# Performance work log

Hardware: AMD Instinct MI355X
Metric: run time of the kernel (lower is better)

Reference implementation:

```python
import jax, jax.numpy as jnp
import numpy as np

B, S, D, H = 8, 1024, 256, 8
DH = D // H
NEG = -1e32


def setup_inputs() -> dict:
    key = jax.random.key(0)
    ks = jax.random.split(key, 8)
    scale = 1.0 / np.sqrt(D)
    return {
        "q": jax.random.normal(ks[0], (B, S, D), jnp.float32),
        "k": jax.random.normal(ks[1], (B, S, D), jnp.float32),
        "v": jax.random.normal(ks[2], (B, S, D), jnp.float32),
        "mask": jnp.tril(jnp.ones((1, 1, S, S), dtype=bool)),
        "Wq": jax.random.normal(ks[3], (D, D), jnp.float32) * scale,
        "bq": jnp.zeros((D,), jnp.float32),
        "Wv": jax.random.normal(ks[4], (D, D), jnp.float32) * scale,
        "bv": jnp.zeros((D,), jnp.float32),
        "Wo": jax.random.normal(ks[5], (D, D), jnp.float32) * scale,
        "bo": jnp.zeros((D,), jnp.float32),
        "gammas": jax.random.normal(ks[6], (H, 1, 1), jnp.float32) * 0.1,
    }


def reference(q, k, v, mask, Wq, bq, Wv, bv, Wo, bo, gammas):
    def split_heads(x):  # [B,S,D] -> [B,H,S,DH]
        return x.reshape(B, S, H, DH).transpose(0, 2, 1, 3)

    # key_query_same=True: key projection shares query weights
    qh = split_heads(q @ Wq.T + bq)
    kh = split_heads(k @ Wq.T + bq)
    vh = split_heads(v @ Wv.T + bv)

    scores = jnp.einsum('bhqd,bhkd->bhqk', qh, kh) / jnp.sqrt(jnp.float32(DH))

    # distance-decay effect (computed on detached softmax of masked scores)
    sp = jax.nn.softmax(jnp.where(mask, scores, NEG), axis=-1)
    distcum = jnp.cumsum(sp, axis=-1)                      # [B,H,S,S]
    disttot = jnp.sum(sp, axis=-1, keepdims=True)          # [B,H,S,1]
    pos = jnp.abs(jnp.arange(S)[None, :] - jnp.arange(S)[:, None]).astype(jnp.float32)
    dist = jnp.sqrt(jnp.clip((disttot - distcum) * pos[None, None], 0.0, None))
    dist = jax.lax.stop_gradient(dist)

    g = -jnp.abs(gammas)[None]                             # [1,H,1,1]
    total_effect = jnp.clip(jnp.exp(g * dist), 1e-5, 1e5)

    scores = scores * total_effect
    scores = jax.nn.softmax(jnp.where(mask, scores, NEG), axis=-1)

    out = jnp.einsum('bhqk,bhkd->bhqd', scores, vh)
    concat = out.transpose(0, 2, 1, 3).reshape(B, S, D)
    output = concat @ Wo.T + bo
    return output, scores
```

## Files before the change

kernel.cpp:

```cpp
#include <hip/hip_runtime.h>
#include <hip/hip_fp16.h>
#include <math.h>

constexpr int Bsz = 8, Ssz = 1024, Dsz = 256, Hn = 8, DHn = 32;
constexpr int SST = 1160;

typedef __attribute__((ext_vector_type(8))) short short8;
typedef __attribute__((ext_vector_type(4))) float floatx4;

#define DEV static __device__ __forceinline__

DEV short f2bf(float f) {
  union { float f; unsigned u; } x; x.f = f;
  return (short)((x.u + 0x7fffu + ((x.u >> 16) & 1u)) >> 16);
}
DEV short f2h(float f) {
  __half h = __float2half(f);
  return *(short*)&h;
}
DEV float wmax(float v) {
#pragma unroll
  for (int off = 32; off > 0; off >>= 1) v = fmaxf(v, __shfl_xor(v, off, 64));
  return v;
}
DEV float wsum(float v) {
#pragma unroll
  for (int off = 32; off > 0; off >>= 1) v += __shfl_xor(v, off, 64);
  return v;
}
DEV float wscan_incl(float v) {
  float x = v;
  const int ln = threadIdx.x & 63;
#pragma unroll
  for (int off = 1; off < 64; off <<= 1) {
    float y = __shfl_up(x, off, 64);
    if (ln >= off) x += y;
  }
  return x;
}

DEV void stage_f32(const float* __restrict__ src, short* dst, int k0, int tid) {
  const int row = tid >> 2, cg = tid & 3;
#pragma unroll
  for (int i = 0; i < 4; ++i) {
    const float4 f = *(const float4*)(src + (size_t)row * 256 + k0 + cg * 16 + i * 4);
    const int g = cg * 2 + (i >> 1);
    const int pg = g ^ (row & 7);
    short4 s; s.x = f2bf(f.x); s.y = f2bf(f.y); s.z = f2bf(f.z); s.w = f2bf(f.w);
    *(short4*)(dst + row * 80 + pg * 8 + (i & 1) * 4) = s;
  }
}
DEV void stage_bf16(const short* __restrict__ src, short* dst, int k0, int tid) {
  const int row = tid >> 2, cg = tid & 3;
#pragma unroll
  for (int i = 0; i < 2; ++i) {
    const short8 s = *(const short8*)(src + (size_t)row * 256 + k0 + cg * 16 + i * 8);
    const int pg = (cg * 2 + i) ^ (row & 7);
    *(short8*)(dst + row * 80 + pg * 8) = s;
  }
}

__global__ __launch_bounds__(256, 4) void proj_qkv(
    const float* __restrict__ qi, const float* __restrict__ ki, const float* __restrict__ vi,
    const float* __restrict__ Wq, const float* __restrict__ bq,
    const float* __restrict__ Wv, const float* __restrict__ bv,
    short* __restrict__ qh, short* __restrict__ kh, short* __restrict__ vt) {
  __shared__ short As[64 * 80];
  __shared__ short Bs[64 * 80];
  const int which = blockIdx.y;
  const float* X = (which == 0) ? qi : (which == 1) ? ki : vi;
  const float* W = (which == 2) ? Wv : Wq;
  const float* bias = (which == 2) ? bv : bq;
  const int tid = threadIdx.x, ln = tid & 63, w = tid >> 6;
  const int lm = ln & 15, qq = ln >> 4;
  const int bm = blockIdx.x & 127, bn = blockIdx.x >> 7;
  const float* Xb = X + (size_t)bm * 64 * 256;
  const float* Wb = W + (size_t)bn * 64 * 256;
  const int moff = (w & 1) * 32, noff = (w >> 1) * 32;
  floatx4 acc[2][2] = {};

  for (int k0 = 0; k0 < 256; k0 += 64) {
    __syncthreads();
    stage_f32(Xb, As, k0, tid);
    stage_f32(Wb, Bs, k0, tid);
    __syncthreads();
#pragma unroll
    for (int ks = 0; ks < 2; ++ks) {
      short8 a[2], b[2];
#pragma unroll
      for (int mt = 0; mt < 2; ++mt) {
        const int row = moff + mt * 16 + lm;
        a[mt] = *(const short8*)(As + row * 80 + ((ks * 4 + qq) ^ (row & 7)) * 8);
      }
#pragma unroll
      for (int nt = 0; nt < 2; ++nt) {
        const int row = noff + nt * 16 + lm;
        b[nt] = *(const short8*)(Bs + row * 80 + ((ks * 4 + qq) ^ (row & 7)) * 8);
      }
#pragma unroll
      for (int mt = 0; mt < 2; ++mt)
#pragma unroll
        for (int nt = 0; nt < 2; ++nt)
          acc[mt][nt] = __builtin_amdgcn_mfma_f32_16x16x32_bf16(a[mt], b[nt], acc[mt][nt], 0, 0, 0);
    }
  }

  short* dst = (which == 0) ? qh : (which == 1) ? kh : vt;
#pragma unroll
  for (int mt = 0; mt < 2; ++mt) {
#pragma unroll
    for (int nt = 0; nt < 2; ++nt) {
      const int n = bn * 64 + noff + nt * 16 + lm;
      const float bval = bias[n];
      const int m0 = bm * 64 + moff + mt * 16 + qq * 4;
      const int h = n >> 5, dh = n & 31;
      if (which <= 1) {
#pragma unroll
        for (int r = 0; r < 4; ++r) {
          const int m = m0 + r, b_ = m >> 10, s = m & 1023;
          dst[(((size_t)(b_ * Hn + h) << 10) + s) * DHn + dh] = f2bf(acc[mt][nt][r] + bval);
        }
      } else {
        const int b_ = m0 >> 10, s0 = m0 & 1023;
        short4 pk;
        pk.x = f2bf(acc[mt][nt][0] + bval);
        pk.y = f2bf(acc[mt][nt][1] + bval);
        pk.z = f2bf(acc[mt][nt][2] + bval);
        pk.w = f2bf(acc[mt][nt][3] + bval);
        *(short4*)(dst + ((size_t)((b_ * Hn + h) * DHn + dh) << 10) + s0) = pk;
      }
    }
  }
}

__global__ __launch_bounds__(256, 4) void proj_out(
    const short* __restrict__ oc, const float* __restrict__ Wo,
    const float* __restrict__ bo, float* __restrict__ out) {
  __shared__ short As[64 * 80];
  __shared__ short Bs[64 * 80];
  const int tid = threadIdx.x, ln = tid & 63, w = tid >> 6;
  const int lm = ln & 15, qq = ln >> 4;
  const int bm = blockIdx.x & 127, bn = blockIdx.x >> 7;
  const short* Xb = oc + (size_t)bm * 64 * 256;
  const float* Wb = Wo + (size_t)bn * 64 * 256;
  const int moff = (w & 1) * 32, noff = (w >> 1) * 32;
  floatx4 acc[2][2] = {};

  for (int k0 = 0; k0 < 256; k0 += 64) {
    __syncthreads();
    stage_bf16(Xb, As, k0, tid);
    stage_f32(Wb, Bs, k0, tid);
    __syncthreads();
#pragma unroll
    for (int ks = 0; ks < 2; ++ks) {
      short8 a[2], b[2];
#pragma unroll
      for (int mt = 0; mt < 2; ++mt) {
        const int row = moff + mt * 16 + lm;
        a[mt] = *(const short8*)(As + row * 80 + ((ks * 4 + qq) ^ (row & 7)) * 8);
      }
#pragma unroll
      for (int nt = 0; nt < 2; ++nt) {
        const int row = noff + nt * 16 + lm;
        b[nt] = *(const short8*)(Bs + row * 80 + ((ks * 4 + qq) ^ (row & 7)) * 8);
      }
#pragma unroll
      for (int mt = 0; mt < 2; ++mt)
#pragma unroll
        for (int nt = 0; nt < 2; ++nt)
          acc[mt][nt] = __builtin_amdgcn_mfma_f32_16x16x32_bf16(a[mt], b[nt], acc[mt][nt], 0, 0, 0);
    }
  }
#pragma unroll
  for (int mt = 0; mt < 2; ++mt)
#pragma unroll
    for (int nt = 0; nt < 2; ++nt) {
      const int n = bn * 64 + noff + nt * 16 + lm;
      const float bval = bo[n];
      const int m0 = bm * 64 + moff + mt * 16 + qq * 4;
#pragma unroll
      for (int r = 0; r < 4; ++r)
        out[(size_t)(m0 + r) * 256 + n] = acc[mt][nt][r] + bval;
    }
}

template <int NP>
DEV void phase2(short* ss, float* shead, int row0, int w, int ln, float g) {
  const int c0 = ln * 4;
  for (int rr = 0; rr < 4; ++rr) {
    const int m = w * 4 + rr;
    const int irow = row0 + m;
    short* srow = ss + m * SST;

    float sv[NP * 4], e[NP * 4];
    float lm1 = -INFINITY;
#pragma unroll
    for (int p = 0; p < NP; ++p) {
      const uint2 u = *(const uint2*)(srow + p * 256 + c0);
      const float2 f0 = __half22float2(*(const __half2*)&u.x);
      const float2 f1 = __half22float2(*(const __half2*)&u.y);
      sv[p * 4 + 0] = f0.x; sv[p * 4 + 1] = f0.y;
      sv[p * 4 + 2] = f1.x; sv[p * 4 + 3] = f1.y;
#pragma unroll
      for (int j = 0; j < 4; ++j)
        if (p * 256 + c0 + j <= irow) lm1 = fmaxf(lm1, sv[p * 4 + j]);
    }
    const float m1 = wmax(lm1);

    float carry = 0.f, excl[NP];
#pragma unroll
    for (int p = 0; p < NP; ++p) {
      float ls = 0.f;
#pragma unroll
      for (int j = 0; j < 4; ++j) {
        const int c = p * 256 + c0 + j;
        e[p * 4 + j] = (c <= irow) ? __expf(sv[p * 4 + j] - m1) : 0.f;
        ls += e[p * 4 + j];
      }
      const float incl = wscan_incl(ls);
      excl[p] = carry + incl - ls;
      carry += __shfl(incl, 63, 64);
    }
    const float Z = carry, invZ = 1.f / Z;

    float lm2 = -INFINITY;
#pragma unroll
    for (int p = 0; p < NP; ++p) {
      float cum = excl[p];
#pragma unroll
      for (int j = 0; j < 4; ++j) {
        const int c = p * 256 + c0 + j;
        cum += e[p * 4 + j];
        const float tail = (Z - cum) * invZ;
        const float pos = (float)(irow - c);
        const float dist = sqrtf(fmaxf(tail * pos, 0.f));
        float eff = __expf(g * dist);
        eff = fminf(fmaxf(eff, 1e-5f), 1e5f);
        const float s2 = sv[p * 4 + j] * eff;
        sv[p * 4 + j] = s2;
        if (c <= irow) lm2 = fmaxf(lm2, s2);
      }
    }
    const float m2 = wmax(lm2);

    float ls2 = 0.f;
#pragma unroll
    for (int p = 0; p < NP; ++p)
#pragma unroll
      for (int j = 0; j < 4; ++j) {
        const int c = p * 256 + c0 + j;
        e[p * 4 + j] = (c <= irow) ? __expf(sv[p * 4 + j] - m2) : 0.f;
        ls2 += e[p * 4 + j];
      }
    const float i2 = 1.f / wsum(ls2);

    float* grow = shead + (size_t)irow * Ssz;
#pragma unroll
    for (int p = 0; p < NP; ++p) {
      float4 o;
      o.x = e[p * 4 + 0] * i2; o.y = e[p * 4 + 1] * i2;
      o.z = e[p * 4 + 2] * i2; o.w = e[p * 4 + 3] * i2;
      *(float4*)(grow + p * 256 + c0) = o;
      uint2 pk;
      pk.x = (uint)(unsigned short)f2bf(o.x) | ((uint)(unsigned short)f2bf(o.y) << 16);
      pk.y = (uint)(unsigned short)f2bf(o.z) | ((uint)(unsigned short)f2bf(o.w) << 16);
      *(uint2*)(srow + p * 256 + c0) = pk;
    }
  }
}

__global__ __launch_bounds__(256, 4) void attn_kernel(
    const short* __restrict__ qh, const short* __restrict__ kh,
    const short* __restrict__ vt, const float* __restrict__ gammas,
    float* __restrict__ scores_out, short* __restrict__ oc) {
  __shared__ short ss[16 * SST];

  const int tid = threadIdx.x, ln = tid & 63, w = tid >> 6;
  const int lm = ln & 15, qq = ln >> 4;
  const int bh = blockIdx.x >> 6;
  const int row0 = (63 - (blockIdx.x & 63)) << 4;
  const int h = bh & 7, b = bh >> 3;
  const float scale = 0.17677669529663687f;
  const float g = -fabsf(gammas[h]);

  const short* qhead = qh + (size_t)bh * Ssz * DHn;
  const short* khead = kh + (size_t)bh * Ssz * DHn;
  const short* vhead = vt + (size_t)bh * DHn * Ssz;
  float* shead = scores_out + ((size_t)bh << 20);

  const short8 qa = *(const short8*)(qhead + (row0 + lm) * DHn + qq * 8);

  const int ntile = (row0 >> 4) + 1;
  for (int t = w; t < ntile; t += 4) {
    const int n0 = t * 16;
    const short8 kb = *(const short8*)(khead + (n0 + lm) * DHn + qq * 8);
    floatx4 c = {0.f, 0.f, 0.f, 0.f};
    c = __builtin_amdgcn_mfma_f32_16x16x32_bf16(qa, kb, c, 0, 0, 0);
#pragma unroll
    for (int r = 0; r < 4; ++r)
      ss[(qq * 4 + r) * SST + n0 + lm] = f2h(c[r] * scale);
  }
  __syncthreads();

  const int NPc = (row0 >> 8) + 1;
  switch (NPc) {
    case 1: phase2<1>(ss, shead, row0, w, ln, g); break;
    case 2: phase2<2>(ss, shead, row0, w, ln, g); break;
    case 3: phase2<3>(ss, shead, row0, w, ln, g); break;
    default: phase2<4>(ss, shead, row0, w, ln, g); break;
  }

  if (NPc < 4) {
    const float4 z4 = make_float4(0.f, 0.f, 0.f, 0.f);
    for (int r = 0; r < 16; ++r) {
      float* grow = shead + (size_t)(row0 + r) * Ssz + NPc * 256;
      for (int i = tid; i < (4 - NPc) * 64; i += 256)
        ((float4*)grow)[i] = z4;
    }
  }
  __syncthreads();

  floatx4 o0 = {0.f, 0.f, 0.f, 0.f}, o1 = {0.f, 0.f, 0.f, 0.f};
  const int nkt = (row0 >> 5) + 1;
  for (int kt = w; kt < nkt; kt += 4) {
    const int k0 = kt * 32;
    const short8 av = *(const short8*)(ss + lm * SST + k0 + qq * 8);
    const short8 b0 = *(const short8*)(vhead + (lm << 10) + k0 + qq * 8);
    const short8 b1 = *(const short8*)(vhead + ((16 + lm) << 10) + k0 + qq * 8);
    o0 = __builtin_amdgcn_mfma_f32_16x16x32_bf16(av, b0, o0, 0, 0, 0);
    o1 = __builtin_amdgcn_mfma_f32_16x16x32_bf16(av, b1, o1, 0, 0, 0);
  }
  __syncthreads();
  float* red = (float*)ss;
#pragma unroll
  for (int r = 0; r < 4; ++r) {
    red[(w * 16 + qq * 4 + r) * 32 + lm] = o0[r];
    red[(w * 16 + qq * 4 + r) * 32 + 16 + lm] = o1[r];
  }
  __syncthreads();
  {
    const int m = tid >> 4, n = tid & 15;
    float a0 = 0.f, a1 = 0.f;
#pragma unroll
    for (int wv = 0; wv < 4; ++wv) {
      a0 += red[(wv * 16 + m) * 32 + n];
      a1 += red[(wv * 16 + m) * 32 + 16 + n];
    }
    const size_t row = ((size_t)b << 10) + row0 + m;
    oc[row * Dsz + h * DHn + n] = f2bf(a0);
    oc[row * Dsz + h * DHn + 16 + n] = f2bf(a1);
  }
}

extern "C" void kernel_launch(void* const* d_in, const int* in_sizes, int n_in,
                              void* d_out, int out_size, void* d_ws, size_t ws_size,
                              hipStream_t stream) {
  const float* q  = (const float*)d_in[0];
  const float* k  = (const float*)d_in[1];
  const float* v  = (const float*)d_in[2];
  const float* Wq = (const float*)d_in[4];
  const float* bq = (const float*)d_in[5];
  const float* Wv = (const float*)d_in[6];
  const float* bv = (const float*)d_in[7];
  const float* Wo = (const float*)d_in[8];
  const float* bo = (const float*)d_in[9];
  const float* gm = (const float*)d_in[10];

  float* out    = (float*)d_out;
  float* scores = out + (size_t)Bsz * Ssz * Dsz;

  const size_t Q = (size_t)Bsz * Hn * Ssz * DHn;
  short* qh = (short*)d_ws;
  short* kh = qh + Q;
  short* vt = kh + Q;
  short* oc = vt + Q;

  const dim3 blk(256);
  hipLaunchKernelGGL(proj_qkv, dim3(512, 3), blk, 0, stream,
                     q, k, v, Wq, bq, Wv, bv, qh, kh, vt);
  hipLaunchKernelGGL(attn_kernel, dim3(Bsz * Hn * (Ssz / 16)), blk, 0, stream,
                     qh, kh, vt, gm, scores, oc);
  hipLaunchKernelGGL(proj_out, dim3(512), blk, 0, stream, oc, Wo, bo, out);
}
```

Before: 395.5 us.

## Pre-pack weights into bf16 MFMA fragments and use non-temporal output stores

Adds a small kernel that converts Wq, Wv and Wo once per call into bf16 fragments laid out in MFMA operand order. The projection GEMMs can then load B operands straight from global memory instead of converting and staging them through LDS. Blocks now cover 32 rows by the full 256 columns. Score and output stores become non-temporal to reduce cache pollution from the large score tensor. The trade-offs are an extra kernel launch and fewer, larger projection blocks.

```diff
diff --git a/kernel.cpp b/kernel.cpp
--- a/kernel.cpp
+++ b/kernel.cpp
@@ -39,82 +39,81 @@
   return x;
 }
 
-DEV void stage_f32(const float* __restrict__ src, short* dst, int k0, int tid) {
-  const int row = tid >> 2, cg = tid & 3;
-#pragma unroll
-  for (int i = 0; i < 4; ++i) {
-    const float4 f = *(const float4*)(src + (size_t)row * 256 + k0 + cg * 16 + i * 4);
-    const int g = cg * 2 + (i >> 1);
-    const int pg = g ^ (row & 7);
-    short4 s; s.x = f2bf(f.x); s.y = f2bf(f.y); s.z = f2bf(f.z); s.w = f2bf(f.w);
-    *(short4*)(dst + row * 80 + pg * 8 + (i & 1) * 4) = s;
-  }
-}
-DEV void stage_bf16(const short* __restrict__ src, short* dst, int k0, int tid) {
-  const int row = tid >> 2, cg = tid & 3;
-#pragma unroll
-  for (int i = 0; i < 2; ++i) {
-    const short8 s = *(const short8*)(src + (size_t)row * 256 + k0 + cg * 16 + i * 8);
-    const int pg = (cg * 2 + i) ^ (row & 7);
-    *(short8*)(dst + row * 80 + pg * 8) = s;
-  }
-}
-
-__global__ __launch_bounds__(256, 4) void proj_qkv(
+__global__ __launch_bounds__(256) void cvt_wfrag(const float* __restrict__ Wq,
+                                                 const float* __restrict__ Wv,
+                                                 const float* __restrict__ Wo,
+                                                 short* __restrict__ dst) {
+  const int which = blockIdx.y;
+  const float* W = (which == 0) ? Wq : (which == 1) ? Wv : Wo;
+  const int t = blockIdx.x * 256 + threadIdx.x;
+  const int ln = t & 63, nt = (t >> 6) & 15, kblk = t >> 10;
+  const float* src = W + (size_t)(nt * 16 + (ln & 15)) * 256 + kblk * 32 + (ln >> 4) * 8;
+  const float4 a = *(const float4*)src;
+  const float4 b = *(const float4*)(src + 4);
+  const float tmp[8] = {a.x, a.y, a.z, a.w, b.x, b.y, b.z, b.w};
+  short8 s;
+#pragma unroll
+  for (int j = 0; j < 8; ++j) s[j] = f2bf(tmp[j]);
+  *(short8*)(dst + ((size_t)which << 16) + (size_t)t * 8) = s;
+}
+
+__global__ __launch_bounds__(256, 4) void proj_qkv2(
     const float* __restrict__ qi, const float* __restrict__ ki, const float* __restrict__ vi,
-    const float* __restrict__ Wq, const float* __restrict__ bq,
-    const float* __restrict__ Wv, const float* __restrict__ bv,
+    const short* __restrict__ Wfrag, const float* __restrict__ bq, const float* __restrict__ bv,
     short* __restrict__ qh, short* __restrict__ kh, short* __restrict__ vt) {
-  __shared__ short As[64 * 80];
-  __shared__ short Bs[64 * 80];
+  __shared__ short Xs[32 * 80];
   const int which = blockIdx.y;
   const float* X = (which == 0) ? qi : (which == 1) ? ki : vi;
-  const float* W = (which == 2) ? Wv : Wq;
+  const short* Wf = Wfrag + ((which == 2) ? (1 << 16) : 0);
   const float* bias = (which == 2) ? bv : bq;
   const int tid = threadIdx.x, ln = tid & 63, w = tid >> 6;
   const int lm = ln & 15, qq = ln >> 4;
-  const int bm = blockIdx.x & 127, bn = blockIdx.x >> 7;
-  const float* Xb = X + (size_t)bm * 64 * 256;
-  const float* Wb = W + (size_t)bn * 64 * 256;
-  const int moff = (w & 1) * 32, noff = (w >> 1) * 32;
-  floatx4 acc[2][2] = {};
-
-  for (int k0 = 0; k0 < 256; k0 += 64) {
+  const int bm = blockIdx.x;
+  const float* Xb = X + (size_t)bm * 32 * 256;
+  floatx4 acc[2][4] = {};
+
+  for (int k0 = 0; k0 < 4; ++k0) {
     __syncthreads();
-    stage_f32(Xb, As, k0, tid);
-    stage_f32(Wb, Bs, k0, tid);
+    {
+      const int row = tid >> 3, cg = tid & 7;
+#pragma unroll
+      for (int i = 0; i < 2; ++i) {
+        const float4 f = *(const float4*)(Xb + (size_t)row * 256 + k0 * 64 + cg * 8 + i * 4);
+        short4 s; s.x = f2bf(f.x); s.y = f2bf(f.y); s.z = f2bf(f.z); s.w = f2bf(f.w);
+        *(short4*)(Xs + row * 80 + (cg ^ (row & 7)) * 8 + i * 4) = s;
+      }
+    }
     __syncthreads();
 #pragma unroll
     for (int ks = 0; ks < 2; ++ks) {
-      short8 a[2], b[2];
+      const int kblk = k0 * 2 + ks;
+      short8 a[2], b[4];
 #pragma unroll
       for (int mt = 0; mt < 2; ++mt) {
-        const int row = moff + mt * 16 + lm;
-        a[mt] = *(const short8*)(As + row * 80 + ((ks * 4 + qq) ^ (row & 7)) * 8);
-      }
-#pragma unroll
-      for (int nt = 0; nt < 2; ++nt) {
-        const int row = noff + nt * 16 + lm;
-        b[nt] = *(const short8*)(Bs + row * 80 + ((ks * 4 + qq) ^ (row & 7)) * 8);
-      }
+        const int row = mt * 16 + lm;
+        a[mt] = *(const short8*)(Xs + row * 80 + (((ks * 4 + qq)) ^ (row & 7)) * 8);
+      }
+#pragma unroll
+      for (int nt = 0; nt < 4; ++nt)
+        b[nt] = *(const short8*)(Wf + ((size_t)(kblk * 16 + w * 4 + nt) * 64 + ln) * 8);
 #pragma unroll
       for (int mt = 0; mt < 2; ++mt)
 #pragma unroll
-        for (int nt = 0; nt < 2; ++nt)
+        for (int nt = 0; nt < 4; ++nt)
           acc[mt][nt] = __builtin_amdgcn_mfma_f32_16x16x32_bf16(a[mt], b[nt], acc[mt][nt], 0, 0, 0);
     }
   }
 
-  short* dst = (which == 0) ? qh : (which == 1) ? kh : vt;
 #pragma unroll
   for (int mt = 0; mt < 2; ++mt) {
 #pragma unroll
-    for (int nt = 0; nt < 2; ++nt) {
-      const int n = bn * 64 + noff + nt * 16 + lm;
+    for (int nt = 0; nt < 4; ++nt) {
+      const int n = w * 64 + nt * 16 + lm;
       const float bval = bias[n];
-      const int m0 = bm * 64 + moff + mt * 16 + qq * 4;
+      const int m0 = bm * 32 + mt * 16 + qq * 4;
       const int h = n >> 5, dh = n & 31;
       if (which <= 1) {
+        short* dst = (which == 0) ? qh : kh;
 #pragma unroll
         for (int r = 0; r < 4; ++r) {
           const int m = m0 + r, b_ = m >> 10, s = m & 1023;
@@ -127,60 +126,60 @@
         pk.y = f2bf(acc[mt][nt][1] + bval);
         pk.z = f2bf(acc[mt][nt][2] + bval);
         pk.w = f2bf(acc[mt][nt][3] + bval);
-        *(short4*)(dst + ((size_t)((b_ * Hn + h) * DHn + dh) << 10) + s0) = pk;
-      }
-    }
-  }
-}
-
-__global__ __launch_bounds__(256, 4) void proj_out(
-    const short* __restrict__ oc, const float* __restrict__ Wo,
+        *(short4*)(vt + ((size_t)((b_ * Hn + h) * DHn + dh) << 10) + s0) = pk;
+      }
+    }
+  }
+}
+
+__global__ __launch_bounds__(256, 4) void proj_out2(
+    const short* __restrict__ oc, const short* __restrict__ Wfrag,
     const float* __restrict__ bo, float* __restrict__ out) {
-  __shared__ short As[64 * 80];
-  __shared__ short Bs[64 * 80];
+  __shared__ short Xs[32 * 80];
+  const short* Wf = Wfrag + (2 << 16);
   const int tid = threadIdx.x, ln = tid & 63, w = tid >> 6;
   const int lm = ln & 15, qq = ln >> 4;
-  const int bm = blockIdx.x & 127, bn = blockIdx.x >> 7;
-  const short* Xb = oc + (size_t)bm * 64 * 256;
-  const float* Wb = Wo + (size_t)bn * 64 * 256;
-  const int moff = (w & 1) * 32, noff = (w >> 1) * 32;
-  floatx4 acc[2][2] = {};
-
-  for (int k0 = 0; k0 < 256; k0 += 64) {
+  const int bm = blockIdx.x;
+  const short* Xb = oc + (size_t)bm * 32 * 256;
+  floatx4 acc[2][4] = {};
+
+  for (int k0 = 0; k0 < 4; ++k0) {
     __syncthreads();
-    stage_bf16(Xb, As, k0, tid);
-    stage_f32(Wb, Bs, k0, tid);
+    {
+      const int row = tid >> 3, cg = tid & 7;
+      const short8 s = *(const short8*)(Xb + (size_t)row * 256 + k0 * 64 + cg * 8);
+      *(short8*)(Xs + row * 80 + (cg ^ (row & 7)) * 8) = s;
+    }
     __syncthreads();
 #pragma unroll
     for (int ks = 0; ks < 2; ++ks) {
-      short8 a[2], b[2];
+      const int kblk = k0 * 2 + ks;
+      short8 a[2], b[4];
 #pragma unroll
       for (int mt = 0; mt < 2; ++mt) {
-        const int row = moff + mt * 16 + lm;
-        a[mt] = *(const short8*)(As + row * 80 + ((ks * 4 + qq) ^ (row & 7)) * 8);
-      }
-#pragma unroll
-      for (int nt = 0; nt < 2; ++nt) {
-        const int row = noff + nt * 16 + lm;
-        b[nt] = *(const short8*)(Bs + row * 80 + ((ks * 4 + qq) ^ (row & 7)) * 8);
-      }
+        const int row = mt * 16 + lm;
+        a[mt] = *(const short8*)(Xs + row * 80 + (((ks * 4 + qq)) ^ (row & 7)) * 8);
+      }
+#pragma unroll
+      for (int nt = 0; nt < 4; ++nt)
+        b[nt] = *(const short8*)(Wf + ((size_t)(kblk * 16 + w * 4 + nt) * 64 + ln) * 8);
 #pragma unroll
       for (int mt = 0; mt < 2; ++mt)
 #pragma unroll
-        for (int nt = 0; nt < 2; ++nt)
+        for (int nt = 0; nt < 4; ++nt)
           acc[mt][nt] = __builtin_amdgcn_mfma_f32_16x16x32_bf16(a[mt], b[nt], acc[mt][nt], 0, 0, 0);
     }
   }
 #pragma unroll
   for (int mt = 0; mt < 2; ++mt)
 #pragma unroll
-    for (int nt = 0; nt < 2; ++nt) {
-      const int n = bn * 64 + noff + nt * 16 + lm;
+    for (int nt = 0; nt < 4; ++nt) {
+      const int n = w * 64 + nt * 16 + lm;
       const float bval = bo[n];
-      const int m0 = bm * 64 + moff + mt * 16 + qq * 4;
+      const int m0 = bm * 32 + mt * 16 + qq * 4;
 #pragma unroll
       for (int r = 0; r < 4; ++r)
-        out[(size_t)(m0 + r) * 256 + n] = acc[mt][nt][r] + bval;
+        __builtin_nontemporal_store(acc[mt][nt][r] + bval, out + (size_t)(m0 + r) * 256 + n);
     }
 }
 
@@ -257,10 +256,10 @@
     float* grow = shead + (size_t)irow * Ssz;
 #pragma unroll
     for (int p = 0; p < NP; ++p) {
-      float4 o;
+      floatx4 o;
       o.x = e[p * 4 + 0] * i2; o.y = e[p * 4 + 1] * i2;
       o.z = e[p * 4 + 2] * i2; o.w = e[p * 4 + 3] * i2;
-      *(float4*)(grow + p * 256 + c0) = o;
+      __builtin_nontemporal_store(o, (floatx4*)(grow + p * 256 + c0));
       uint2 pk;
       pk.x = (uint)(unsigned short)f2bf(o.x) | ((uint)(unsigned short)f2bf(o.y) << 16);
       pk.y = (uint)(unsigned short)f2bf(o.z) | ((uint)(unsigned short)f2bf(o.w) << 16);
@@ -311,11 +310,11 @@
   }
 
   if (NPc < 4) {
-    const float4 z4 = make_float4(0.f, 0.f, 0.f, 0.f);
+    const floatx4 z4 = {0.f, 0.f, 0.f, 0.f};
     for (int r = 0; r < 16; ++r) {
       float* grow = shead + (size_t)(row0 + r) * Ssz + NPc * 256;
       for (int i = tid; i < (4 - NPc) * 64; i += 256)
-        ((float4*)grow)[i] = z4;
+        __builtin_nontemporal_store(z4, ((floatx4*)grow) + i);
     }
   }
   __syncthreads();
@@ -374,11 +373,13 @@
   short* kh = qh + Q;
   short* vt = kh + Q;
   short* oc = vt + Q;
+  short* Wf = oc + Q;
 
   const dim3 blk(256);
-  hipLaunchKernelGGL(proj_qkv, dim3(512, 3), blk, 0, stream,
-                     q, k, v, Wq, bq, Wv, bv, qh, kh, vt);
+  hipLaunchKernelGGL(cvt_wfrag, dim3(32, 3), blk, 0, stream, Wq, Wv, Wo, Wf);
+  hipLaunchKernelGGL(proj_qkv2, dim3(256, 3), blk, 0, stream,
+                     q, k, v, Wf, bq, bv, qh, kh, vt);
   hipLaunchKernelGGL(attn_kernel, dim3(Bsz * Hn * (Ssz / 16)), blk, 0, stream,
                      qh, kh, vt, gm, scores, oc);
-  hipLaunchKernelGGL(proj_out, dim3(512), blk, 0, stream, oc, Wo, bo, out);
-}
+  hipLaunchKernelGGL(proj_out2, dim3(256), blk, 0, stream, oc, Wf, bo, out);
+}
```

After: 381.2 us. -3.6%, faster.
